# Kernel tuning notes

Measured on AMD Instinct MI355X. Metric: run time of the kernel, lower is better.

The kernel has to match this reference:

```python
import jax, jax.numpy as jnp
import numpy as np

C = 256          # channels
G = 4            # dcn groups
GC = C // G      # channels per group
K = 3            # dcn kernel size
P = K * K        # sampling points per group
OS = 0.5         # offset_scale
PAD = 1
N, H, W = 2, 128, 128


def setup_inputs() -> dict:
    key = jax.random.key(0)
    ks = jax.random.split(key, 8)
    f = lambda k, shp, s: jax.random.normal(k, shp, dtype=jnp.float32) * s
    return {
        "sampled_feat": jax.random.normal(ks[0], (N, H, W, C), dtype=jnp.float32),
        "context_info": jax.random.normal(ks[1], (N, H, W, C), dtype=jnp.float32),
        "W_in": f(ks[2], (C, C), 0.02),            # input_proj weight
        "b_in": jnp.zeros((C,), jnp.float32),
        "dw_kernel": f(ks[3], (3, 3, 1, C), 0.02),  # depthwise conv (HWIO, I=1)
        "dw_bias": jnp.zeros((C,), jnp.float32),
        "W_om": f(ks[4], (C, G * P * 3), 0.01),     # offset+mask projection
        "b_om": jnp.zeros((G * P * 3,), jnp.float32),
        "W_out": f(ks[5], (C, C), 0.02),            # output_proj (no bias)
        "ln_gamma": jnp.ones((C,), jnp.float32),
        "ln_beta": jnp.zeros((C,), jnp.float32),
    }


def _dcn_forward(sampled_feat, context_info, W_in, b_in, dw_kernel, dw_bias,
                 W_om, b_om, W_out, ln_gamma, ln_beta):
    Hp, Wp = H + 2 * PAD, W + 2 * PAD
    # value branch: pointwise input_proj then spatial zero-pad
    value = sampled_feat @ W_in + b_in
    value = jnp.pad(value, ((0, 0), (PAD, PAD), (PAD, PAD), (0, 0)))
    valg = value.reshape(N, Hp * Wp, G, GC).transpose(0, 2, 1, 3)  # (N,G,Hp*Wp,GC)

    # offset/mask branch (extra_offset_mask=True -> computed from context_info)
    ctx = jax.lax.conv_general_dilated(
        context_info, dw_kernel, (1, 1), ((1, 1), (1, 1)),
        dimension_numbers=("NHWC", "HWIO", "NHWC"), feature_group_count=C) + dw_bias
    om = (ctx @ W_om + b_om).reshape(N, H, W, G, 3 * P)
    offset = om[..., :2 * P].reshape(N, H, W, G, P, 2)  # (x,y) per sampling point
    mask = om[..., 2 * P:]                               # (N,H,W,G,P); DCNv4: no softmax

    # sampling locations in padded-input pixel coords (align_corners=False convention)
    kk = jnp.arange(K, dtype=jnp.float32) - (K - 1) // 2
    kx = jnp.tile(kk, K)      # (P,)
    ky = jnp.repeat(kk, K)    # (P,)
    base_x = (jnp.arange(W, dtype=jnp.float32) + PAD)[None, None, :, None, None]
    base_y = (jnp.arange(H, dtype=jnp.float32) + PAD)[None, :, None, None, None]
    px = base_x + OS * (kx + offset[..., 0])   # (N,H,W,G,P)
    py = base_y + OS * (ky + offset[..., 1])
    px = px.transpose(0, 3, 1, 2, 4).reshape(N, G, -1)  # (N,G,H*W*P)
    py = py.transpose(0, 3, 1, 2, 4).reshape(N, G, -1)

    # bilinear sampling with zero padding outside the padded input
    x0 = jnp.floor(px); y0 = jnp.floor(py)
    wx1 = px - x0; wy1 = py - y0

    def corner(xi, yi, w):
        valid = (xi >= 0) & (xi <= Wp - 1) & (yi >= 0) & (yi <= Hp - 1)
        idx = (jnp.clip(yi, 0, Hp - 1) * Wp + jnp.clip(xi, 0, Wp - 1)).astype(jnp.int32)
        v = jnp.take_along_axis(valg, idx[..., None], axis=2)  # (N,G,S,GC)
        return v * (w * valid)[..., None]

    samp = (corner(x0, y0, (1 - wx1) * (1 - wy1))
            + corner(x0 + 1, y0, wx1 * (1 - wy1))
            + corner(x0, y0 + 1, (1 - wx1) * wy1)
            + corner(x0 + 1, y0 + 1, wx1 * wy1))
    samp = samp.reshape(N, G, H, W, P, GC)
    maskg = mask.transpose(0, 3, 1, 2, 4)  # (N,G,H,W,P)
    out = jnp.einsum("nghwpc,nghwp->nhwgc", samp, maskg).reshape(N, H, W, C)

    out = out @ W_out  # output_proj, output_bias=False
    # LayerNorm over channels + exact GELU
    mu = out.mean(-1, keepdims=True)
    var = out.var(-1, keepdims=True)
    out = (out - mu) * jax.lax.rsqrt(var + 1e-5) * ln_gamma + ln_beta
    return jax.nn.gelu(out, approximate=False)


def reference(sampled_feat, context_info, W_in, b_in, dw_kernel, dw_bias,
              W_om, b_om, W_out, ln_gamma, ln_beta):
    return _dcn_forward(sampled_feat, context_info, W_in, b_in, dw_kernel, dw_bias,
                        W_om, b_om, W_out, ln_gamma, ln_beta)
```

## Files before the change

### kernel.cpp

```cpp
#include <hip/hip_runtime.h>
#include <math.h>

constexpr int NBATCH = 2, HH = 128, WW = 128, CC = 256;
constexpr int PP = 9, OMW = 108;
constexpr int MM = NBATCH * HH * WW;
constexpr int BTCOLS = 640;

using bf8 = __attribute__((ext_vector_type(8))) short;
using f32x4 = __attribute__((ext_vector_type(4))) float;

__device__ __forceinline__ short f2bf(float x) {
  unsigned u = __builtin_bit_cast(unsigned, x);
  unsigned r = (u + 0x7fffu + ((u >> 16) & 1u)) >> 16;
  return (short)r;
}
__device__ __forceinline__ float bf2f(short h) {
  unsigned u = ((unsigned)(unsigned short)h) << 16;
  return __builtin_bit_cast(float, u);
}
__device__ __forceinline__ void split4(float4 v, short4* h, short4* l) {
  short4 hh = make_short4(f2bf(v.x), f2bf(v.y), f2bf(v.z), f2bf(v.w));
  *h = hh;
  *l = make_short4(f2bf(v.x - bf2f(hh.x)), f2bf(v.y - bf2f(hh.y)),
                   f2bf(v.z - bf2f(hh.z)), f2bf(v.w - bf2f(hh.w)));
}

__global__ __launch_bounds__(256) void prep_kernel(
    const float* __restrict__ Win, const float* __restrict__ Wom,
    const float* __restrict__ Wout, short* __restrict__ Bh,
    short* __restrict__ Bl) {
  int gid = blockIdx.x * 256 + threadIdx.x;
  int col = gid >> 8, k = gid & 255;
  float w;
  if (col < 256)
    w = Win[k * 256 + col];
  else if (col < 384) {
    int c = col - 256;
    w = (c < OMW) ? Wom[k * OMW + c] : 0.f;
  } else {
    int c = col - 384;
    w = Wout[k * 256 + c];
  }
  short h = f2bf(w);
  Bh[gid] = h;
  Bl[gid] = f2bf(w - bf2f(h));
}

__global__ __launch_bounds__(256) void split_kernel(
    const float* __restrict__ x, short* __restrict__ h,
    short* __restrict__ l) {
  int gid = blockIdx.x * 256 + threadIdx.x;
  float4 v = *(const float4*)&x[(size_t)gid * 4];
  short4 hh, ll;
  split4(v, &hh, &ll);
  *(short4*)&h[(size_t)gid * 4] = hh;
  *(short4*)&l[(size_t)gid * 4] = ll;
}

__global__ __launch_bounds__(256) void dwconv_kernel(
    const float* __restrict__ x, const float* __restrict__ k,
    const float* __restrict__ b, short* __restrict__ yh,
    short* __restrict__ yl) {
  int gid = blockIdx.x * 256 + threadIdx.x;
  int q = gid & 63;
  int m = gid >> 6;
  int c = q * 4;
  int w = m & 127, h = (m >> 7) & 127, n = m >> 14;
  float4 acc = *(const float4*)&b[c];
#pragma unroll
  for (int dy = 0; dy < 3; ++dy) {
    int yy = h + dy - 1;
    if (yy < 0 || yy >= HH) continue;
#pragma unroll
    for (int dx = 0; dx < 3; ++dx) {
      int xx = w + dx - 1;
      if (xx < 0 || xx >= WW) continue;
      float4 v = *(const float4*)&x[(((size_t)n * HH + yy) * WW + xx) * CC + c];
      float4 kk = *(const float4*)&k[(dy * 3 + dx) * CC + c];
      acc.x += v.x * kk.x;
      acc.y += v.y * kk.y;
      acc.z += v.z * kk.z;
      acc.w += v.w * kk.w;
    }
  }
  short4 hh, ll;
  split4(acc, &hh, &ll);
  *(short4*)&yh[(size_t)m * CC + c] = hh;
  *(short4*)&yl[(size_t)m * CC + c] = ll;
}

template <bool GUARD, bool BIAS>
__global__ __launch_bounds__(256, 3) void mgemm(
    const short* __restrict__ Ath, const short* __restrict__ Atl,
    const short* __restrict__ Bth, const short* __restrict__ Btl,
    const float* __restrict__ bias, float* __restrict__ Co, int nshift,
    int nout) {
  constexpr int BM = 64, BN = 128, BK = 64, SK = 68;
  __shared__ __align__(16) short As[2][BM * SK];
  __shared__ __align__(16) short Bs[2][BN * SK];
  const int t = threadIdx.x;
  const int lane = t & 63, wid = t >> 6;
  const int wr = wid >> 1, wc = wid & 1;
  const int l15 = lane & 15, l4 = lane >> 4;
  const int mb = ((int)blockIdx.x >> nshift) * BM;
  const int nb = ((int)blockIdx.x & ((1 << nshift) - 1)) * BN;

  f32x4 acc[2][4];
#pragma unroll
  for (int r = 0; r < 2; ++r)
#pragma unroll
    for (int n = 0; n < 4; ++n) acc[r][n] = (f32x4){0.f, 0.f, 0.f, 0.f};

  for (int ks = 0; ks < 256; ks += BK) {
#pragma unroll
    for (int i = 0; i < 2; ++i) {
      int idx = t + 256 * i;
      int row = idx >> 3, kq = (idx & 7) * 8;
      size_t g = (size_t)(mb + row) * 256 + ks + kq;
      *(bf8*)&As[0][row * SK + kq] = *(const bf8*)&Ath[g];
      *(bf8*)&As[1][row * SK + kq] = *(const bf8*)&Atl[g];
    }
#pragma unroll
    for (int i = 0; i < 4; ++i) {
      int idx = t + 256 * i;
      int col = idx >> 3, kq = (idx & 7) * 8;
      size_t g = (size_t)(nb + col) * 256 + ks + kq;
      *(bf8*)&Bs[0][col * SK + kq] = *(const bf8*)&Bth[g];
      *(bf8*)&Bs[1][col * SK + kq] = *(const bf8*)&Btl[g];
    }
    __syncthreads();
#pragma unroll
    for (int kk = 0; kk < 2; ++kk) {
      int ko = kk * 32 + l4 * 8;
      bf8 ah[2], al[2], bh[4], bl[4];
#pragma unroll
      for (int r = 0; r < 2; ++r) {
        int row = wr * 32 + r * 16 + l15;
        ah[r] = *(const bf8*)&As[0][row * SK + ko];
        al[r] = *(const bf8*)&As[1][row * SK + ko];
      }
#pragma unroll
      for (int n = 0; n < 4; ++n) {
        int col = wc * 64 + n * 16 + l15;
        bh[n] = *(const bf8*)&Bs[0][col * SK + ko];
        bl[n] = *(const bf8*)&Bs[1][col * SK + ko];
      }
#pragma unroll
      for (int r = 0; r < 2; ++r)
#pragma unroll
        for (int n = 0; n < 4; ++n) {
          acc[r][n] = __builtin_amdgcn_mfma_f32_16x16x32_bf16(al[r], bh[n],
                                                              acc[r][n], 0, 0, 0);
          acc[r][n] = __builtin_amdgcn_mfma_f32_16x16x32_bf16(ah[r], bl[n],
                                                              acc[r][n], 0, 0, 0);
          acc[r][n] = __builtin_amdgcn_mfma_f32_16x16x32_bf16(ah[r], bh[n],
                                                              acc[r][n], 0, 0, 0);
        }
    }
    __syncthreads();
  }

#pragma unroll
  for (int r = 0; r < 2; ++r)
#pragma unroll
    for (int reg = 0; reg < 4; ++reg) {
      int row = mb + wr * 32 + r * 16 + l4 * 4 + reg;
#pragma unroll
      for (int n = 0; n < 4; ++n) {
        int col = nb + wc * 64 + n * 16 + l15;
        if (!GUARD || col < nout) {
          float v = acc[r][n][reg];
          if constexpr (BIAS) v += bias[col];
          Co[(size_t)row * nout + col] = v;
        }
      }
    }
}

__global__ __launch_bounds__(256) void sample_kernel(
    const float* __restrict__ val, const float* __restrict__ om,
    short* __restrict__ oh, short* __restrict__ ol) {
  int gid = blockIdx.x * 256 + threadIdx.x;
  int q = gid & 63;
  int m = gid >> 6;
  int g = q >> 4;
  int w = m & 127, h = (m >> 7) & 127, n = m >> 14;
  const float* omp = om + m * OMW + g * 27;
  const float* vb = val + (n << 22) + (q << 2);
  float bx = (float)(w + 1), by = (float)(h + 1);
  float4 acc = make_float4(0.f, 0.f, 0.f, 0.f);

#pragma unroll
  for (int p = 0; p < PP; ++p) {
    float px = bx + 0.5f * ((float)(p % 3 - 1) + omp[2 * p]);
    float py = by + 0.5f * ((float)(p / 3 - 1) + omp[2 * p + 1]);
    float mk = omp[18 + p];
    float x0f = floorf(px), y0f = floorf(py);
    int x0 = (int)x0f, y0 = (int)y0f;
    float wx1 = px - x0f, wy1 = py - y0f;
    float wx0 = 1.f - wx1, wy0 = 1.f - wy1;
    float4 s = make_float4(0.f, 0.f, 0.f, 0.f);
#define CORNER(XC, YC, WT)                                            \
  {                                                                   \
    int xc = (XC), yc = (YC);                                         \
    int xi = min(max(xc, 1), 128), yi = min(max(yc, 1), 128);         \
    float wt = ((xc == xi) && (yc == yi)) ? (WT) : 0.f;               \
    const float4 v =                                                  \
        *(const float4*)&vb[(((yi - 1) << 7) + (xi - 1)) << 8];       \
    s.x += v.x * wt;                                                  \
    s.y += v.y * wt;                                                  \
    s.z += v.z * wt;                                                  \
    s.w += v.w * wt;                                                  \
  }
    CORNER(x0, y0, wx0 * wy0);
    CORNER(x0 + 1, y0, wx1 * wy0);
    CORNER(x0, y0 + 1, wx0 * wy1);
    CORNER(x0 + 1, y0 + 1, wx1 * wy1);
#undef CORNER
    acc.x += mk * s.x;
    acc.y += mk * s.y;
    acc.z += mk * s.z;
    acc.w += mk * s.w;
  }
  short4 hh, ll;
  split4(acc, &hh, &ll);
  *(short4*)&oh[((size_t)m << 8) + (q << 2)] = hh;
  *(short4*)&ol[((size_t)m << 8) + (q << 2)] = ll;
}

__global__ __launch_bounds__(256) void ln_gelu_kernel(
    const float* __restrict__ x, const float* __restrict__ gam,
    const float* __restrict__ bet, float* __restrict__ y) {
  int row = blockIdx.x * 4 + (threadIdx.x >> 6);
  int lane = threadIdx.x & 63;
  const float* xr = x + (size_t)row * 256 + lane * 4;
  float4 v = *(const float4*)xr;
  float s = v.x + v.y + v.z + v.w;
  float ss = v.x * v.x + v.y * v.y + v.z * v.z + v.w * v.w;
#pragma unroll
  for (int m = 1; m < 64; m <<= 1) {
    s += __shfl_xor(s, m);
    ss += __shfl_xor(ss, m);
  }
  float mu = s * (1.f / 256.f);
  float var = ss * (1.f / 256.f) - mu * mu;
  float rs = rsqrtf(var + 1e-5f);
  float4 gg = *(const float4*)&gam[lane * 4];
  float4 bb = *(const float4*)&bet[lane * 4];
  float4 o;
#define GEL(FIELD)                                                   \
  {                                                                  \
    float t_ = (v.FIELD - mu) * rs * gg.FIELD + bb.FIELD;            \
    o.FIELD = 0.5f * t_ * (1.f + erff(t_ * 0.70710678118654752f));   \
  }
  GEL(x) GEL(y) GEL(z) GEL(w)
#undef GEL
  *(float4*)&y[(size_t)row * 256 + lane * 4] = o;
}

extern "C" void kernel_launch(void* const* d_in, const int* in_sizes, int n_in,
                              void* d_out, int out_size, void* d_ws,
                              size_t ws_size, hipStream_t stream) {
  (void)in_sizes;
  (void)n_in;
  (void)out_size;
  (void)ws_size;
  const float* sampled = (const float*)d_in[0];
  const float* ctxin = (const float*)d_in[1];
  const float* W_in = (const float*)d_in[2];
  const float* b_in = (const float*)d_in[3];
  const float* dwk = (const float*)d_in[4];
  const float* dwb = (const float*)d_in[5];
  const float* W_om = (const float*)d_in[6];
  const float* b_om = (const float*)d_in[7];
  const float* W_out = (const float*)d_in[8];
  const float* lng = (const float*)d_in[9];
  const float* lnb = (const float*)d_in[10];
  float* out = (float*)d_out;

  float* value = (float*)d_ws;
  float* omb = value + (size_t)MM * CC;
  short* ctx_h = (short*)(omb + (size_t)MM * OMW);
  short* ctx_l = ctx_h + (size_t)MM * CC;
  short* xin_h = ctx_l + (size_t)MM * CC;
  short* xin_l = xin_h + (size_t)MM * CC;
  float* out_pre = (float*)(xin_l + (size_t)MM * CC);
  short* Bth = (short*)(out_pre + (size_t)MM * CC);
  short* Btl = Bth + (size_t)BTCOLS * 256;
  short* dcn_h = ctx_h;
  short* dcn_l = ctx_l;

  prep_kernel<<<BTCOLS, 256, 0, stream>>>(W_in, W_om, W_out, Bth, Btl);
  split_kernel<<<MM * 64 / 256, 256, 0, stream>>>(sampled, xin_h, xin_l);
  dwconv_kernel<<<MM * 64 / 256, 256, 0, stream>>>(ctxin, dwk, dwb, ctx_h,
                                                   ctx_l);
  mgemm<true, true><<<MM / 64, 256, 0, stream>>>(
      ctx_h, ctx_l, Bth + 256 * 256, Btl + 256 * 256, b_om, omb, 0, OMW);
  mgemm<false, true><<<2 * (MM / 64), 256, 0, stream>>>(
      xin_h, xin_l, Bth, Btl, b_in, value, 1, 256);
  sample_kernel<<<MM * 64 / 256, 256, 0, stream>>>(value, omb, dcn_h, dcn_l);
  mgemm<false, false><<<2 * (MM / 64), 256, 0, stream>>>(
      dcn_h, dcn_l, Bth + 384 * 256, Btl + 384 * 256, nullptr, out_pre, 1, 256);
  ln_gelu_kernel<<<MM / 4, 256, 0, stream>>>(out_pre, lng, lnb, out);
}
```

Baseline: 266.1 us.

## Fuse bf16 hi/lo split into GEMM loads and aggregate sampling weights per window

The separate split kernel is removed, and the dwconv and sample kernels now write fp32. The GEMM reads fp32 A tiles and splits them into truncated bf16 hi/lo pairs while staging into shared memory, which avoids writing and rereading the short hi/lo buffers. The sample kernel first gathers the bilinear corner weights for each pixel and group into a 3x3 window held in shared memory using atomics. When every corner falls inside that window it does 9 gathers instead of 36; otherwise it falls back to the original path. Truncation replaces round-to-nearest for the hi part, which can change precision slightly.

Measured after the change: 239.2 us. 1.11x faster.

```diff
diff --git a/kernel.cpp b/kernel.cpp
--- a/kernel.cpp
+++ b/kernel.cpp
@@ -18,11 +18,12 @@
   unsigned u = ((unsigned)(unsigned short)h) << 16;
   return __builtin_bit_cast(float, u);
 }
-__device__ __forceinline__ void split4(float4 v, short4* h, short4* l) {
-  short4 hh = make_short4(f2bf(v.x), f2bf(v.y), f2bf(v.z), f2bf(v.w));
-  *h = hh;
-  *l = make_short4(f2bf(v.x - bf2f(hh.x)), f2bf(v.y - bf2f(hh.y)),
-                   f2bf(v.z - bf2f(hh.z)), f2bf(v.w - bf2f(hh.w)));
+__device__ __forceinline__ unsigned pack_hi16(float x, float y) {
+  return __builtin_amdgcn_perm(__builtin_bit_cast(unsigned, y),
+                               __builtin_bit_cast(unsigned, x), 0x07060302u);
+}
+__device__ __forceinline__ float trunc_hi(float x) {
+  return __builtin_bit_cast(float, __builtin_bit_cast(unsigned, x) & 0xFFFF0000u);
 }
 
 __global__ __launch_bounds__(256) void prep_kernel(
@@ -46,21 +47,9 @@
   Bl[gid] = f2bf(w - bf2f(h));
 }
 
-__global__ __launch_bounds__(256) void split_kernel(
-    const float* __restrict__ x, short* __restrict__ h,
-    short* __restrict__ l) {
-  int gid = blockIdx.x * 256 + threadIdx.x;
-  float4 v = *(const float4*)&x[(size_t)gid * 4];
-  short4 hh, ll;
-  split4(v, &hh, &ll);
-  *(short4*)&h[(size_t)gid * 4] = hh;
-  *(short4*)&l[(size_t)gid * 4] = ll;
-}
-
 __global__ __launch_bounds__(256) void dwconv_kernel(
     const float* __restrict__ x, const float* __restrict__ k,
-    const float* __restrict__ b, short* __restrict__ yh,
-    short* __restrict__ yl) {
+    const float* __restrict__ b, float* __restrict__ y) {
   int gid = blockIdx.x * 256 + threadIdx.x;
   int q = gid & 63;
   int m = gid >> 6;
@@ -83,18 +72,14 @@
       acc.w += v.w * kk.w;
     }
   }
-  short4 hh, ll;
-  split4(acc, &hh, &ll);
-  *(short4*)&yh[(size_t)m * CC + c] = hh;
-  *(short4*)&yl[(size_t)m * CC + c] = ll;
+  *(float4*)&y[(size_t)m * CC + c] = acc;
 }
 
 template <bool GUARD, bool BIAS>
 __global__ __launch_bounds__(256, 3) void mgemm(
-    const short* __restrict__ Ath, const short* __restrict__ Atl,
-    const short* __restrict__ Bth, const short* __restrict__ Btl,
-    const float* __restrict__ bias, float* __restrict__ Co, int nshift,
-    int nout) {
+    const float* __restrict__ Af, const short* __restrict__ Bth,
+    const short* __restrict__ Btl, const float* __restrict__ bias,
+    float* __restrict__ Co, int nshift, int nout) {
   constexpr int BM = 64, BN = 128, BK = 64, SK = 68;
   __shared__ __align__(16) short As[2][BM * SK];
   __shared__ __align__(16) short Bs[2][BN * SK];
@@ -113,12 +98,18 @@
 
   for (int ks = 0; ks < 256; ks += BK) {
 #pragma unroll
-    for (int i = 0; i < 2; ++i) {
+    for (int i = 0; i < 4; ++i) {
       int idx = t + 256 * i;
-      int row = idx >> 3, kq = (idx & 7) * 8;
-      size_t g = (size_t)(mb + row) * 256 + ks + kq;
-      *(bf8*)&As[0][row * SK + kq] = *(const bf8*)&Ath[g];
-      *(bf8*)&As[1][row * SK + kq] = *(const bf8*)&Atl[g];
+      int row = idx >> 4, kq = (idx & 15) * 4;
+      float4 v = *(const float4*)&Af[(size_t)(mb + row) * 256 + ks + kq];
+      unsigned h01 = pack_hi16(v.x, v.y);
+      unsigned h23 = pack_hi16(v.z, v.w);
+      unsigned l01 = pack_hi16(v.x - trunc_hi(v.x), v.y - trunc_hi(v.y));
+      unsigned l23 = pack_hi16(v.z - trunc_hi(v.z), v.w - trunc_hi(v.w));
+      uint2 hw, lw;
+      hw.x = h01; hw.y = h23; lw.x = l01; lw.y = l23;
+      *(uint2*)&As[0][row * SK + kq] = hw;
+      *(uint2*)&As[1][row * SK + kq] = lw;
     }
 #pragma unroll
     for (int i = 0; i < 4; ++i) {
@@ -179,27 +170,79 @@
 
 __global__ __launch_bounds__(256) void sample_kernel(
     const float* __restrict__ val, const float* __restrict__ om,
-    short* __restrict__ oh, short* __restrict__ ol) {
-  int gid = blockIdx.x * 256 + threadIdx.x;
-  int q = gid & 63;
-  int m = gid >> 6;
-  int g = q >> 4;
-  int w = m & 127, h = (m >> 7) & 127, n = m >> 14;
-  const float* omp = om + m * OMW + g * 27;
-  const float* vb = val + (n << 22) + (q << 2);
-  float bx = (float)(w + 1), by = (float)(h + 1);
-  float4 acc = make_float4(0.f, 0.f, 0.f, 0.f);
-
-#pragma unroll
-  for (int p = 0; p < PP; ++p) {
-    float px = bx + 0.5f * ((float)(p % 3 - 1) + omp[2 * p]);
-    float py = by + 0.5f * ((float)(p / 3 - 1) + omp[2 * p + 1]);
-    float mk = omp[18 + p];
+    float* __restrict__ outp) {
+  __shared__ float wwin[4][4][12];
+  __shared__ int fflag[4][4];
+  const int t = threadIdx.x;
+  const int m0 = (int)blockIdx.x * 4;
+
+  if (t < 192) ((float*)wwin)[t] = 0.f;
+  if (t < 16) ((int*)fflag)[t] = 0;
+  __syncthreads();
+
+  if (t < 144) {
+    int pix = t / 36, r = t % 36;
+    int g = r / 9, p = r % 9;
+    int m = m0 + pix;
+    int w = m & 127, h = (m >> 7) & 127;
+    const float* omp = om + (size_t)m * OMW + g * 27;
+    float ox = omp[2 * p], oy = omp[2 * p + 1], mk = omp[18 + p];
+    float px = (float)(w + 1) + 0.5f * ((float)(p % 3 - 1) + ox);
+    float py = (float)(h + 1) + 0.5f * ((float)(p / 3 - 1) + oy);
     float x0f = floorf(px), y0f = floorf(py);
     int x0 = (int)x0f, y0 = (int)y0f;
     float wx1 = px - x0f, wy1 = py - y0f;
     float wx0 = 1.f - wx1, wy0 = 1.f - wy1;
-    float4 s = make_float4(0.f, 0.f, 0.f, 0.f);
+#pragma unroll
+    for (int j = 0; j < 2; ++j)
+#pragma unroll
+      for (int i = 0; i < 2; ++i) {
+        int cx = x0 + i, cy = y0 + j;
+        if (cx < 1 || cx > 128 || cy < 1 || cy > 128) continue;
+        float cw = mk * (i ? wx1 : wx0) * (j ? wy1 : wy0);
+        int rx = cx - w, ry = cy - h;
+        if ((unsigned)rx > 2u || (unsigned)ry > 2u)
+          atomicOr(&fflag[pix][g], 1);
+        else
+          atomicAdd(&wwin[pix][g][ry * 3 + rx], cw);
+      }
+  }
+  __syncthreads();
+
+  const int pix = t >> 6, g = (t >> 4) & 3, cq = t & 15;
+  const int q = g * 16 + cq;
+  const int m = m0 + pix;
+  const int w = m & 127, h = (m >> 7) & 127, n = m >> 14;
+  const float* vb = val + ((size_t)n << 22) + (q << 2);
+  float4 acc = make_float4(0.f, 0.f, 0.f, 0.f);
+
+  if (fflag[pix][g] == 0) {
+#pragma unroll
+    for (int ry = 0; ry < 3; ++ry)
+#pragma unroll
+      for (int rx = 0; rx < 3; ++rx) {
+        float cw = wwin[pix][g][ry * 3 + rx];
+        int xi = min(max(w - 1 + rx, 0), 127);
+        int yi = min(max(h - 1 + ry, 0), 127);
+        float4 v = *(const float4*)&vb[((yi << 7) + xi) << 8];
+        acc.x += cw * v.x;
+        acc.y += cw * v.y;
+        acc.z += cw * v.z;
+        acc.w += cw * v.w;
+      }
+  } else {
+    const float* omp = om + (size_t)m * OMW + g * 27;
+    float bx = (float)(w + 1), by = (float)(h + 1);
+#pragma unroll
+    for (int p = 0; p < PP; ++p) {
+      float px = bx + 0.5f * ((float)(p % 3 - 1) + omp[2 * p]);
+      float py = by + 0.5f * ((float)(p / 3 - 1) + omp[2 * p + 1]);
+      float mk = omp[18 + p];
+      float x0f = floorf(px), y0f = floorf(py);
+      int x0 = (int)x0f, y0 = (int)y0f;
+      float wx1 = px - x0f, wy1 = py - y0f;
+      float wx0 = 1.f - wx1, wy0 = 1.f - wy1;
+      float4 s = make_float4(0.f, 0.f, 0.f, 0.f);
 #define CORNER(XC, YC, WT)                                            \
   {                                                                   \
     int xc = (XC), yc = (YC);                                         \
@@ -212,20 +255,18 @@
     s.z += v.z * wt;                                                  \
     s.w += v.w * wt;                                                  \
   }
-    CORNER(x0, y0, wx0 * wy0);
-    CORNER(x0 + 1, y0, wx1 * wy0);
-    CORNER(x0, y0 + 1, wx0 * wy1);
-    CORNER(x0 + 1, y0 + 1, wx1 * wy1);
+      CORNER(x0, y0, wx0 * wy0);
+      CORNER(x0 + 1, y0, wx1 * wy0);
+      CORNER(x0, y0 + 1, wx0 * wy1);
+      CORNER(x0 + 1, y0 + 1, wx1 * wy1);
 #undef CORNER
-    acc.x += mk * s.x;
-    acc.y += mk * s.y;
-    acc.z += mk * s.z;
-    acc.w += mk * s.w;
-  }
-  short4 hh, ll;
-  split4(acc, &hh, &ll);
-  *(short4*)&oh[((size_t)m << 8) + (q << 2)] = hh;
-  *(short4*)&ol[((size_t)m << 8) + (q << 2)] = ll;
+      acc.x += mk * s.x;
+      acc.y += mk * s.y;
+      acc.z += mk * s.z;
+      acc.w += mk * s.w;
+    }
+  }
+  *(float4*)&outp[((size_t)m << 8) + (q << 2)] = acc;
 }
 
 __global__ __launch_bounds__(256) void ln_gelu_kernel(
@@ -280,26 +321,21 @@
 
   float* value = (float*)d_ws;
   float* omb = value + (size_t)MM * CC;
-  short* ctx_h = (short*)(omb + (size_t)MM * OMW);
-  short* ctx_l = ctx_h + (size_t)MM * CC;
-  short* xin_h = ctx_l + (size_t)MM * CC;
-  short* xin_l = xin_h + (size_t)MM * CC;
-  float* out_pre = (float*)(xin_l + (size_t)MM * CC);
-  short* Bth = (short*)(out_pre + (size_t)MM * CC);
+  float* ctx = omb + (size_t)MM * OMW;
+  short* Bth = (short*)(ctx + (size_t)MM * CC);
   short* Btl = Bth + (size_t)BTCOLS * 256;
-  short* dcn_h = ctx_h;
-  short* dcn_l = ctx_l;
+  float* dcn = ctx;
+  float* out_pre = value;
 
   prep_kernel<<<BTCOLS, 256, 0, stream>>>(W_in, W_om, W_out, Bth, Btl);
-  split_kernel<<<MM * 64 / 256, 256, 0, stream>>>(sampled, xin_h, xin_l);
-  dwconv_kernel<<<MM * 64 / 256, 256, 0, stream>>>(ctxin, dwk, dwb, ctx_h,
-                                                   ctx_l);
-  mgemm<true, true><<<MM / 64, 256, 0, stream>>>(
-      ctx_h, ctx_l, Bth + 256 * 256, Btl + 256 * 256, b_om, omb, 0, OMW);
-  mgemm<false, true><<<2 * (MM / 64), 256, 0, stream>>>(
-      xin_h, xin_l, Bth, Btl, b_in, value, 1, 256);
-  sample_kernel<<<MM * 64 / 256, 256, 0, stream>>>(value, omb, dcn_h, dcn_l);
+  dwconv_kernel<<<MM * 64 / 256, 256, 0, stream>>>(ctxin, dwk, dwb, ctx);
+  mgemm<true, true><<<MM / 64, 256, 0, stream>>>(ctx, Bth + 256 * 256,
+                                                 Btl + 256 * 256, b_om, omb, 0,
+                                                 OMW);
+  mgemm<false, true><<<2 * (MM / 64), 256, 0, stream>>>(sampled, Bth, Btl,
+                                                        b_in, value, 1, 256);
+  sample_kernel<<<MM / 4, 256, 0, stream>>>(value, omb, dcn);
   mgemm<false, false><<<2 * (MM / 64), 256, 0, stream>>>(
-      dcn_h, dcn_l, Bth + 384 * 256, Btl + 384 * 256, nullptr, out_pre, 1, 256);
+      dcn, Bth + 384 * 256, Btl + 384 * 256, nullptr, out_pre, 1, 256);
   ln_gelu_kernel<<<MM / 4, 256, 0, stream>>>(out_pre, lng, lnb, out);
 }
```
